# Performance work log

Measured on AMD Instinct MI355X. Metric: run time of the kernel, lower is better.

Reference implementation:

```python
import jax, jax.numpy as jnp
import numpy as np

B, N, E = 8, 10000, 160000
F_IN, HID, EMB = 5, 128, 256
A_LAST, S_STEP = 10, 1


def _gcn_layer(x, src, dst, W, b, num_nodes):
    # PyG GCNConv: h = x @ W^T, add self-loops, symmetric norm, scatter-add, + bias
    h = x @ W.T
    loops = jnp.arange(num_nodes, dtype=src.dtype)
    src2 = jnp.concatenate([src, loops])
    dst2 = jnp.concatenate([dst, loops])
    deg = jax.ops.segment_sum(jnp.ones_like(dst2, dtype=h.dtype), dst2, num_segments=num_nodes)
    dinv = jnp.where(deg > 0, jax.lax.rsqrt(deg), 0.0)
    norm = dinv[src2] * dinv[dst2]                     # [E+N]
    msgs = h[src2] * norm[:, None]                     # gather + scale
    out = jax.ops.segment_sum(msgs, dst2, num_segments=num_nodes)
    return out + b


def setup_inputs() -> dict:
    key = jax.random.key(0)
    ks = jax.random.split(key, 14)
    graph_x = jax.random.normal(ks[0], (B, N, F_IN), dtype=jnp.float32)
    graph_edges = jax.random.randint(ks[1], (B, 2, E), 0, N, dtype=jnp.int64)
    position_seq = jax.random.randint(ks[2], (B,), 0, N, dtype=jnp.int64)
    available_moves = jax.random.randint(ks[3], (B, 4), 0, N, dtype=jnp.int64)
    actions = jax.random.normal(ks[4], (B, A_LAST), dtype=jnp.float32)
    steps = jax.random.normal(ks[5], (B, S_STEP), dtype=jnp.float32)

    def glorot(k, shape):
        fan_in = shape[-1]
        return jax.random.normal(k, shape, dtype=jnp.float32) / jnp.sqrt(jnp.float32(fan_in))

    proj_in = HID * 5 + A_LAST + S_STEP
    params = {
        'W1': glorot(ks[6], (HID, F_IN)), 'b1': jnp.zeros((HID,), jnp.float32),
        'W2': glorot(ks[7], (HID, HID)), 'b2': jnp.zeros((HID,), jnp.float32),
        'Wp1': glorot(ks[8], (EMB, proj_in)), 'bp1': jnp.zeros((EMB,), jnp.float32),
        'Wp2': glorot(ks[9], (EMB, EMB)), 'bp2': jnp.zeros((EMB,), jnp.float32),
    }
    return dict(graph_x=graph_x, graph_edges=graph_edges, position_seq=position_seq,
                available_moves=available_moves, actions=actions, steps=steps, **params)


def reference(graph_x, graph_edges, position_seq, available_moves, actions, steps,
              W1, b1, W2, b2, Wp1, bp1, Wp2, bp2):
    b, n, f = graph_x.shape
    num_nodes = b * n
    x = graph_x.reshape(num_nodes, f)
    addition = (jnp.arange(b, dtype=graph_edges.dtype) * n)
    ei = graph_edges + addition[:, None, None]          # [B,2,E]
    ei = jnp.swapaxes(ei, 0, 1).reshape(2, -1)          # [2, B*E]
    src, dst = ei[0], ei[1]
    position = position_seq + addition
    all_positions = jnp.concatenate(
        [available_moves + addition[:, None], position[:, None]], axis=1)  # [B,5]

    x = jax.nn.relu(_gcn_layer(x, src, dst, W1, b1, num_nodes))
    x = jax.nn.relu(_gcn_layer(x, src, dst, W2, b2, num_nodes))

    current_x = x[all_positions].reshape(b, -1)          # [B, 5*HID]
    current_x = jnp.concatenate([current_x, actions, steps], axis=-1)
    h = jax.nn.relu(current_x @ Wp1.T + bp1)
    return h @ Wp2.T + bp2
```

## Files before the change

kernel.cpp:

```cpp
#include <hip/hip_runtime.h>

#define NB 8
#define NN 10000
#define NE 160000
#define NNODES (NB*NN)
#define NEDGE (NB*NE)
#define FIN 5
#define HID 128
#define EMB 256
#define ALAST 10
#define PROJ_IN (HID*5 + ALAST + 1)
#define NPOS 40
#define E0CAP 256
#define TCAP (NPOS + NPOS*E0CAP)

#define C_NT 0
#define C_E0(t) (8 + (t)*16)

__global__ void k_mark(const int* __restrict__ avail, const int* __restrict__ pos,
                       int* __restrict__ markT, int* __restrict__ Tnodes,
                       int* __restrict__ cnts,
                       int* __restrict__ pos2t0, int* __restrict__ posNode) {
    int p = threadIdx.x;
    int n = 0;
    if (p < NPOS) {
        int b = p / 5, pi = p - b*5;
        int node = (pi < 4) ? avail[b*4 + pi] : pos[b];
        n = node + b*NN;
    }
    int firstIdx = p;
    for (int q = 0; q < NPOS; ++q) {
        int nq = __shfl(n, q, 64);
        if (p < NPOS && q < p && nq == n && firstIdx == p) firstIdx = q;
    }
    bool isFirst = (p < NPOS) && (firstIdx == p);
    unsigned long long bal = __ballot(isFirst);
    if (p < NPOS) {
        int slot = __popcll(bal & ((1ull << firstIdx) - 1ull));
        if (isFirst) {
            markT[n] = slot; Tnodes[slot] = n;
        }
        pos2t0[p] = slot; posNode[p] = n;
    }
    if (p == 0) cnts[C_NT] = __popcll(bal);
}

__global__ __launch_bounds__(256) void k_pass1(const int* __restrict__ edges,
        const int* __restrict__ markT, int* __restrict__ cnts,
        int* __restrict__ e0) {
    int idx = blockIdx.x*256 + threadIdx.x;
    int g = idx / (NE/4), w4 = idx - g*(NE/4);
    const int* base = edges + (size_t)g*2*NE;
    int4 d4 = ((const int4*)(base + NE))[w4];
    int gofs = g*NN;
    int dd[4] = {d4.x, d4.y, d4.z, d4.w};
    #pragma unroll
    for (int c = 0; c < 4; ++c) {
        int t0 = markT[gofs + dd[c]];
        if (t0 >= 0) {
            int s = base[4*w4 + c] + gofs;
            int k = atomicAdd(&cnts[C_E0(t0)], 1);
            if (k < E0CAP) e0[t0*E0CAP + k] = s;
        }
    }
}

__global__ __launch_bounds__(256) void k_dedup(const int* __restrict__ e0,
                        int* __restrict__ cnts, int* __restrict__ markT,
                        int* __restrict__ Tnodes) {
    __shared__ int lc, base;
    int t0 = blockIdx.x;
    if (threadIdx.x == 0) lc = 0;
    __syncthreads();
    int m = cnts[C_E0(t0)]; if (m > E0CAP) m = E0CAP;
    int s = -1, myIdx = -1;
    if ((int)threadIdx.x < m) {
        s = e0[t0*E0CAP + threadIdx.x];
        if (atomicCAS(&markT[s], -1, -2) == -1)
            myIdx = atomicAdd(&lc, 1);
    }
    __syncthreads();
    if (threadIdx.x == 0 && lc > 0) base = atomicAdd(&cnts[C_NT], lc);
    __syncthreads();
    if (myIdx >= 0) {
        int slot = base + myIdx;
        Tnodes[slot] = s;
        markT[s] = slot;
    }
}

__global__ __launch_bounds__(256) void k_pass2a(const int* __restrict__ edges,
        int* __restrict__ markT) {
    int idx = blockIdx.x*256 + threadIdx.x;
    int g = idx / (NE/4), w4 = idx - g*(NE/4);
    const int* base = edges + (size_t)g*2*NE;
    int4 d4 = ((const int4*)(base + NE))[w4];
    int gofs = g*NN;
    int dd[4] = {d4.x, d4.y, d4.z, d4.w};
    #pragma unroll
    for (int c = 0; c < 4; ++c) {
        if (markT[gofs + dd[c]] >= 0) {
            int s = base[4*w4 + c] + gofs;
            if (markT[s] == -1) markT[s] = -3;
        }
    }
}

__global__ __launch_bounds__(256) void k_pass3(const int* __restrict__ edges,
        const int* __restrict__ markT, int* __restrict__ degCnt) {
    int idx = blockIdx.x*256 + threadIdx.x;
    int g = idx / (NE/4), w4 = idx - g*(NE/4);
    int4 d4 = ((const int4*)(edges + (size_t)g*2*NE + NE))[w4];
    int gofs = g*NN;
    int dd[4] = {d4.x, d4.y, d4.z, d4.w};
    #pragma unroll
    for (int c = 0; c < 4; ++c) {
        int n = gofs + dd[c];
        if (markT[n] != -1) atomicAdd(&degCnt[n], 1);
    }
}

__global__ __launch_bounds__(256) void k_pass2b(const int* __restrict__ edges,
        const int* __restrict__ markT, const int* __restrict__ degCnt,
        const float* __restrict__ xg, float* __restrict__ axT) {
    int idx = blockIdx.x*256 + threadIdx.x;
    int g = idx / (NE/4), w4 = idx - g*(NE/4);
    const int* base = edges + (size_t)g*2*NE;
    int4 d4 = ((const int4*)(base + NE))[w4];
    int gofs = g*NN;
    int dd[4] = {d4.x, d4.y, d4.z, d4.w};
    #pragma unroll
    for (int c = 0; c < 4; ++c) {
        int ts = markT[gofs + dd[c]];
        if (ts >= 0) {
            int s = base[4*w4 + c] + gofs;
            float dv = rsqrtf(1.0f + (float)degCnt[s]);
            const float* xr = xg + (size_t)s*FIN;
            float* at = axT + (size_t)ts*FIN;
            #pragma unroll
            for (int f = 0; f < FIN; ++f) unsafeAtomicAdd(&at[f], xr[f]*dv);
        }
    }
}

#define KC 32
__global__ __launch_bounds__(256) void k_h12T(
        const float* __restrict__ axT, const int* __restrict__ Tnodes,
        const int* __restrict__ degCnt, const int* __restrict__ cnts,
        const float* __restrict__ xg,
        const float* __restrict__ W1, const float* __restrict__ b1,
        const float* __restrict__ W2, float* __restrict__ hsT) {
    __shared__ float axs[FIN][128];
    __shared__ float w1s[FIN][128];
    __shared__ float b1s[128];
    __shared__ float dvs[128];
    __shared__ float xs[KC*128];
    __shared__ float wt[KC*64];
    int ntv = cnts[C_NT]; if (ntv > TCAP) ntv = TCAP;
    int jb  = blockIdx.x & 1;
    int m0g = (blockIdx.x >> 1) * 128;
    if (m0g >= ntv) return;
    int tid = threadIdx.x;
    if (tid < 128) {
        b1s[tid] = b1[tid];
        #pragma unroll
        for (int f = 0; f < FIN; ++f) w1s[f][tid] = W1[tid*FIN + f];
    } else {
        int r2 = tid - 128;
        int row = m0g + r2;
        int ok = row < ntv;
        int node = ok ? Tnodes[row] : 0;
        float dvv = ok ? rsqrtf(1.0f + (float)degCnt[node]) : 0.0f;
        dvs[r2] = dvv;
        #pragma unroll
        for (int f = 0; f < FIN; ++f)
            axs[f][r2] = axT[(size_t)row*FIN + f] + xg[(size_t)node*FIN + f]*dvv;
    }
    int tx = tid & 15, ty = tid >> 4;
    int m0 = ty*8;
    int j0 = tx*4;
    int r  = tid >> 1;
    int kq = (tid & 1) * 16;
    int rw  = tid >> 2;
    int kqw = (tid & 3) * 8;
    float a[8][4];
    #pragma unroll
    for (int i = 0; i < 8; ++i)
        #pragma unroll
        for (int j = 0; j < 4; ++j) a[i][j] = 0.f;
    __syncthreads();
    float axr[FIN];
    float dvr = dvs[r];
    #pragma unroll
    for (int f = 0; f < FIN; ++f) axr[f] = axs[f][r] * dvr;

    for (int kh = 0; kh < 128; kh += KC) {
        float4 wv0 = *(const float4*)&W2[(size_t)(jb*64 + rw)*128 + kh + kqw];
        float4 wv1 = *(const float4*)&W2[(size_t)(jb*64 + rw)*128 + kh + kqw + 4];
        float hv[16];
        #pragma unroll
        for (int kk = 0; kk < 16; ++kk) {
            int k1 = kh + kq + kk;
            float sv = b1s[k1];
            #pragma unroll
            for (int f = 0; f < FIN; ++f) sv += axr[f]*w1s[f][k1];
            hv[kk] = fmaxf(sv, 0.0f);
        }
        __syncthreads();
        #pragma unroll
        for (int kk = 0; kk < 16; ++kk) xs[(kq+kk)*128 + r] = hv[kk];
        wt[(kqw+0)*64 + rw] = wv0.x;
        wt[(kqw+1)*64 + rw] = wv0.y;
        wt[(kqw+2)*64 + rw] = wv0.z;
        wt[(kqw+3)*64 + rw] = wv0.w;
        wt[(kqw+4)*64 + rw] = wv1.x;
        wt[(kqw+5)*64 + rw] = wv1.y;
        wt[(kqw+6)*64 + rw] = wv1.z;
        wt[(kqw+7)*64 + rw] = wv1.w;
        __syncthreads();
        for (int k = 0; k < KC; ++k) {
            float4 xa = *(const float4*)&xs[k*128 + m0];
            float4 xb = *(const float4*)&xs[k*128 + m0 + 4];
            float4 wa = *(const float4*)&wt[k*64 + j0];
            float xr[8] = {xa.x,xa.y,xa.z,xa.w,xb.x,xb.y,xb.z,xb.w};
            #pragma unroll
            for (int i = 0; i < 8; ++i) {
                a[i][0] += xr[i]*wa.x;
                a[i][1] += xr[i]*wa.y;
                a[i][2] += xr[i]*wa.z;
                a[i][3] += xr[i]*wa.w;
            }
        }
    }
    #pragma unroll
    for (int i = 0; i < 8; ++i) {
        int row = m0g + m0 + i;
        if (row < ntv) {
            float dv = dvs[m0 + i];
            float4 v0 = make_float4(a[i][0]*dv, a[i][1]*dv, a[i][2]*dv, a[i][3]*dv);
            *(float4*)&hsT[(size_t)row*HID + jb*64 + j0] = v0;
        }
    }
}

__global__ __launch_bounds__(128) void k_aggPT(
        const int* __restrict__ pos2t0, const int* __restrict__ posNode,
        const int* __restrict__ cnts, const int* __restrict__ e0,
        const int* __restrict__ markT, const float* __restrict__ hsT,
        const int* __restrict__ degCnt, const float* __restrict__ b2,
        float* __restrict__ cx40) {
    int p = blockIdx.x;
    int f = threadIdx.x;
    int n = posNode[p];
    int t0 = pos2t0[p];
    float acc = hsT[(size_t)t0*HID + f];
    int m = cnts[C_E0(t0)]; if (m > E0CAP) m = E0CAP;
    for (int j = 0; j < m; ++j) {
        int s = e0[t0*E0CAP + j];
        int ts = markT[s];
        if (ts >= 0) acc += hsT[(size_t)ts*HID + f];
    }
    float dv = rsqrtf(1.0f + (float)degCnt[n]);
    cx40[(size_t)p*HID + f] = fmaxf(acc*dv + b2[f], 0.0f);
}

__global__ __launch_bounds__(256) void k_mlp1(
        const float* __restrict__ cx40, const float* __restrict__ actions,
        const float* __restrict__ steps,
        const float* __restrict__ Wp1, const float* __restrict__ bp1,
        float* __restrict__ hm) {
    int b  = blockIdx.x >> 4;
    int jg = blockIdx.x & 15;
    int t  = threadIdx.x;
    __shared__ float c[PROJ_IN];
    for (int i = t; i < 5*HID; i += 256)
        c[i] = cx40[(size_t)b*5*HID + i];
    if (t < ALAST) c[5*HID + t] = actions[b*ALAST + t];
    if (t == ALAST) c[5*HID + ALAST] = steps[b];
    __syncthreads();
    int o = t >> 4, sub = t & 15;
    int j = jg*16 + o;
    const float* wr = Wp1 + (size_t)j*PROJ_IN;
    float s = 0.f;
    for (int k = sub; k < PROJ_IN; k += 16) s += c[k]*wr[k];
    #pragma unroll
    for (int d = 8; d; d >>= 1) s += __shfl_down(s, d, 16);
    if (sub == 0) hm[b*EMB + j] = fmaxf(s + bp1[j], 0.f);
}

__global__ __launch_bounds__(256) void k_mlp2(
        const float* __restrict__ hm, const float* __restrict__ Wp2,
        const float* __restrict__ bp2, float* __restrict__ out) {
    int b  = blockIdx.x >> 4;
    int jg = blockIdx.x & 15;
    int t  = threadIdx.x;
    __shared__ float c[EMB];
    if (t < EMB) c[t] = hm[b*EMB + t];
    __syncthreads();
    int o = t >> 4, sub = t & 15;
    int j = jg*16 + o;
    const float* wr = Wp2 + (size_t)j*EMB;
    float s = 0.f;
    for (int k = sub; k < EMB; k += 16) s += c[k]*wr[k];
    #pragma unroll
    for (int d = 8; d; d >>= 1) s += __shfl_down(s, d, 16);
    if (sub == 0) out[b*EMB + j] = s + bp2[j];
}

extern "C" void kernel_launch(void* const* d_in, const int* in_sizes, int n_in,
                              void* d_out, int out_size, void* d_ws, size_t ws_size,
                              hipStream_t stream) {
    const float* graph_x = (const float*)d_in[0];
    const int*   edges   = (const int*)d_in[1];
    const int*   pos     = (const int*)d_in[2];
    const int*   avail   = (const int*)d_in[3];
    const float* actions = (const float*)d_in[4];
    const float* steps   = (const float*)d_in[5];
    const float* W1  = (const float*)d_in[6];
    const float* b1  = (const float*)d_in[7];
    const float* W2  = (const float*)d_in[8];
    const float* b2  = (const float*)d_in[9];
    const float* Wp1 = (const float*)d_in[10];
    const float* bp1 = (const float*)d_in[11];
    const float* Wp2 = (const float*)d_in[12];
    const float* bp2 = (const float*)d_in[13];
    float* out = (float*)d_out;

    char* ws = (char*)d_ws;
    size_t off = 0;
    #define ALLOC(ptrname, type, nelem) \
        type* ptrname = (type*)(ws + off); off = (off + (size_t)(nelem)*sizeof(type) + 255) & ~(size_t)255;
    ALLOC(markT,   int,   NNODES)
    ALLOC(degCnt,  int,   NNODES)
    ALLOC(cnts,    int,   1024)
    ALLOC(axT,     float, (size_t)(TCAP+128)*FIN)
    char* msB_end = ws + off;
    ALLOC(Tnodes,  int,   TCAP)
    ALLOC(pos2t0,  int,   NPOS)
    ALLOC(posNode, int,   NPOS)
    ALLOC(e0,      int,   NPOS*E0CAP)
    ALLOC(hsT,     float, (size_t)TCAP*HID)
    ALLOC(cx40,    float, (size_t)NPOS*HID)
    ALLOC(hm,      float, (size_t)NB*EMB)
    #undef ALLOC

    hipMemsetAsync(markT, 0xFF, (size_t)NNODES*4, stream);
    hipMemsetAsync(degCnt, 0x00, (size_t)(msB_end - (char*)degCnt), stream);

    k_mark<<<1, 64, 0, stream>>>(avail, pos, markT, Tnodes, cnts, pos2t0, posNode);
    k_pass1<<<NEDGE/4/256, 256, 0, stream>>>(edges, markT, cnts, e0);
    k_dedup<<<NPOS, 256, 0, stream>>>(e0, cnts, markT, Tnodes);
    k_pass2a<<<NEDGE/4/256, 256, 0, stream>>>(edges, markT);
    k_pass3<<<NEDGE/4/256, 256, 0, stream>>>(edges, markT, degCnt);
    k_pass2b<<<NEDGE/4/256, 256, 0, stream>>>(edges, markT, degCnt, graph_x, axT);
    k_h12T<<<2*((TCAP+127)/128), 256, 0, stream>>>(axT, Tnodes, degCnt, cnts,
                                                   graph_x, W1, b1, W2, hsT);
    k_aggPT<<<NPOS, 128, 0, stream>>>(pos2t0, posNode, cnts, e0, markT, hsT,
                                      degCnt, b2, cx40);
    k_mlp1<<<NB*16, 256, 0, stream>>>(cx40, actions, steps, Wp1, bp1, hm);
    k_mlp2<<<NB*16, 256, 0, stream>>>(hm, Wp2, bp2, out);
}
```

Measured before the change: 173.1 us.

## Record incoming-edge lists in pass2 and drop separate atomic aggregation pass

The edge-scan pass that marks 2-hop neighbours now also appends each in-neighbour's source to a per-target adjacency list, capped at E1C entries. Layer-1 aggregation is then done as a gather loop inside k_h12T instead of a separate full edge pass doing float atomics. This removes one full read of the edge array and the scattered atomics. In exchange it adds an int atomic counter per edge, an e1 buffer, and serial per-row gather loops. The aggregation in k_aggPT also switches from e0 to the e1 lists.

New measurement: 177.5 us. 1.03x slower.

```diff
diff --git a/kernel.cpp b/kernel.cpp
--- a/kernel.cpp
+++ b/kernel.cpp
@@ -13,6 +13,7 @@
 #define NPOS 40
 #define E0CAP 256
 #define TCAP (NPOS + NPOS*E0CAP)
+#define E1C 128
 
 #define C_NT 0
 #define C_E0(t) (8 + (t)*16)
@@ -89,8 +90,8 @@
     }
 }
 
-__global__ __launch_bounds__(256) void k_pass2a(const int* __restrict__ edges,
-        int* __restrict__ markT) {
+__global__ __launch_bounds__(256) void k_pass2(const int* __restrict__ edges,
+        int* __restrict__ markT, int* __restrict__ e1cnt, int* __restrict__ e1) {
     int idx = blockIdx.x*256 + threadIdx.x;
     int g = idx / (NE/4), w4 = idx - g*(NE/4);
     const int* base = edges + (size_t)g*2*NE;
@@ -99,8 +100,11 @@
     int dd[4] = {d4.x, d4.y, d4.z, d4.w};
     #pragma unroll
     for (int c = 0; c < 4; ++c) {
-        if (markT[gofs + dd[c]] >= 0) {
+        int ts = markT[gofs + dd[c]];
+        if (ts >= 0) {
             int s = base[4*w4 + c] + gofs;
+            int k = atomicAdd(&e1cnt[ts*4], 1);
+            if (k < E1C) e1[(size_t)ts*E1C + k] = s;
             if (markT[s] == -1) markT[s] = -3;
         }
     }
@@ -120,32 +124,10 @@
     }
 }
 
-__global__ __launch_bounds__(256) void k_pass2b(const int* __restrict__ edges,
-        const int* __restrict__ markT, const int* __restrict__ degCnt,
-        const float* __restrict__ xg, float* __restrict__ axT) {
-    int idx = blockIdx.x*256 + threadIdx.x;
-    int g = idx / (NE/4), w4 = idx - g*(NE/4);
-    const int* base = edges + (size_t)g*2*NE;
-    int4 d4 = ((const int4*)(base + NE))[w4];
-    int gofs = g*NN;
-    int dd[4] = {d4.x, d4.y, d4.z, d4.w};
-    #pragma unroll
-    for (int c = 0; c < 4; ++c) {
-        int ts = markT[gofs + dd[c]];
-        if (ts >= 0) {
-            int s = base[4*w4 + c] + gofs;
-            float dv = rsqrtf(1.0f + (float)degCnt[s]);
-            const float* xr = xg + (size_t)s*FIN;
-            float* at = axT + (size_t)ts*FIN;
-            #pragma unroll
-            for (int f = 0; f < FIN; ++f) unsafeAtomicAdd(&at[f], xr[f]*dv);
-        }
-    }
-}
-
 #define KC 32
 __global__ __launch_bounds__(256) void k_h12T(
-        const float* __restrict__ axT, const int* __restrict__ Tnodes,
+        const int* __restrict__ e1cnt, const int* __restrict__ e1,
+        const int* __restrict__ Tnodes,
         const int* __restrict__ degCnt, const int* __restrict__ cnts,
         const float* __restrict__ xg,
         const float* __restrict__ W1, const float* __restrict__ b1,
@@ -172,9 +154,22 @@
         int node = ok ? Tnodes[row] : 0;
         float dvv = ok ? rsqrtf(1.0f + (float)degCnt[node]) : 0.0f;
         dvs[r2] = dvv;
-        #pragma unroll
-        for (int f = 0; f < FIN; ++f)
-            axs[f][r2] = axT[(size_t)row*FIN + f] + xg[(size_t)node*FIN + f]*dvv;
+        float acc[FIN];
+        #pragma unroll
+        for (int f = 0; f < FIN; ++f) acc[f] = xg[(size_t)node*FIN + f]*dvv;
+        if (ok) {
+            int m = e1cnt[row*4]; if (m > E1C) m = E1C;
+            const int* lp = e1 + (size_t)row*E1C;
+            for (int j = 0; j < m; ++j) {
+                int s = lp[j];
+                float dv = rsqrtf(1.0f + (float)degCnt[s]);
+                const float* xr = xg + (size_t)s*FIN;
+                #pragma unroll
+                for (int f = 0; f < FIN; ++f) acc[f] += xr[f]*dv;
+            }
+        }
+        #pragma unroll
+        for (int f = 0; f < FIN; ++f) axs[f][r2] = acc[f];
     }
     int tx = tid & 15, ty = tid >> 4;
     int m0 = ty*8;
@@ -245,7 +240,7 @@
 
 __global__ __launch_bounds__(128) void k_aggPT(
         const int* __restrict__ pos2t0, const int* __restrict__ posNode,
-        const int* __restrict__ cnts, const int* __restrict__ e0,
+        const int* __restrict__ e1cnt, const int* __restrict__ e1,
         const int* __restrict__ markT, const float* __restrict__ hsT,
         const int* __restrict__ degCnt, const float* __restrict__ b2,
         float* __restrict__ cx40) {
@@ -254,9 +249,9 @@
     int n = posNode[p];
     int t0 = pos2t0[p];
     float acc = hsT[(size_t)t0*HID + f];
-    int m = cnts[C_E0(t0)]; if (m > E0CAP) m = E0CAP;
+    int m = e1cnt[t0*4]; if (m > E1C) m = E1C;
     for (int j = 0; j < m; ++j) {
-        int s = e0[t0*E0CAP + j];
+        int s = e1[(size_t)t0*E1C + j];
         int ts = markT[s];
         if (ts >= 0) acc += hsT[(size_t)ts*HID + f];
     }
@@ -333,12 +328,13 @@
     ALLOC(markT,   int,   NNODES)
     ALLOC(degCnt,  int,   NNODES)
     ALLOC(cnts,    int,   1024)
-    ALLOC(axT,     float, (size_t)(TCAP+128)*FIN)
+    ALLOC(e1cnt,   int,   TCAP*4)
     char* msB_end = ws + off;
     ALLOC(Tnodes,  int,   TCAP)
     ALLOC(pos2t0,  int,   NPOS)
     ALLOC(posNode, int,   NPOS)
     ALLOC(e0,      int,   NPOS*E0CAP)
+    ALLOC(e1,      int,   (size_t)TCAP*E1C)
     ALLOC(hsT,     float, (size_t)TCAP*HID)
     ALLOC(cx40,    float, (size_t)NPOS*HID)
     ALLOC(hm,      float, (size_t)NB*EMB)
@@ -350,12 +346,11 @@
     k_mark<<<1, 64, 0, stream>>>(avail, pos, markT, Tnodes, cnts, pos2t0, posNode);
     k_pass1<<<NEDGE/4/256, 256, 0, stream>>>(edges, markT, cnts, e0);
     k_dedup<<<NPOS, 256, 0, stream>>>(e0, cnts, markT, Tnodes);
-    k_pass2a<<<NEDGE/4/256, 256, 0, stream>>>(edges, markT);
+    k_pass2<<<NEDGE/4/256, 256, 0, stream>>>(edges, markT, e1cnt, e1);
     k_pass3<<<NEDGE/4/256, 256, 0, stream>>>(edges, markT, degCnt);
-    k_pass2b<<<NEDGE/4/256, 256, 0, stream>>>(edges, markT, degCnt, graph_x, axT);
-    k_h12T<<<2*((TCAP+127)/128), 256, 0, stream>>>(axT, Tnodes, degCnt, cnts,
+    k_h12T<<<2*((TCAP+127)/128), 256, 0, stream>>>(e1cnt, e1, Tnodes, degCnt, cnts,
                                                    graph_x, W1, b1, W2, hsT);
-    k_aggPT<<<NPOS, 128, 0, stream>>>(pos2t0, posNode, cnts, e0, markT, hsT,
+    k_aggPT<<<NPOS, 128, 0, stream>>>(pos2t0, posNode, e1cnt, e1, markT, hsT,
                                       degCnt, b2, cx40);
     k_mlp1<<<NB*16, 256, 0, stream>>>(cx40, actions, steps, Wp1, bp1, hm);
     k_mlp2<<<NB*16, 256, 0, stream>>>(hm, Wp2, bp2, out);
```
